# Kernel tuning notes

Hardware: AMD Instinct MI355X
Metric: run time of the kernel (lower is better)

## Reference

```python
import jax, jax.numpy as jnp
import numpy as np

N = 50000
E = 800000
HEADS = 4
C = 64  # per-head channels
IN = 256
NEG_SLOPE = 0.2


def setup_inputs() -> dict:
    key = jax.random.key(0)
    k = jax.random.split(key, 6)
    x = jax.random.normal(k[0], (N, IN), dtype=jnp.float32)
    edge_index = jax.random.randint(k[1], (2, E), 0, N, dtype=jnp.int64)
    # Glorot-ish scale for weights
    W = jax.random.normal(k[2], (IN, HEADS * C), dtype=jnp.float32) * (1.0 / np.sqrt(IN))
    att_src = jax.random.normal(k[3], (HEADS, C), dtype=jnp.float32) * (1.0 / np.sqrt(C))
    att_dst = jax.random.normal(k[4], (HEADS, C), dtype=jnp.float32) * (1.0 / np.sqrt(C))
    bias = jax.random.normal(k[5], (HEADS * C,), dtype=jnp.float32) * 0.02
    return {"x": x, "edge_index": edge_index, "W": W, "att_src": att_src,
            "att_dst": att_dst, "bias": bias}


def _gat_forward(x, edge_index, W, att_src, att_dst, bias):
    n = x.shape[0]
    h = (x @ W).reshape(n, HEADS, C)  # [N, H, C]

    # add self loops (PyG default add_self_loops=True)
    loop = jnp.arange(n, dtype=edge_index.dtype)
    src = jnp.concatenate([edge_index[0], loop])  # [E+N]
    dst = jnp.concatenate([edge_index[1], loop])

    # per-node attention contributions  [N, H]
    a_src = jnp.einsum('nhc,hc->nh', h, att_src)
    a_dst = jnp.einsum('nhc,hc->nh', h, att_dst)

    # edge logits with leaky relu  [E+N, H]
    logits = a_src[src] + a_dst[dst]
    logits = jnp.where(logits >= 0, logits, NEG_SLOPE * logits)

    # segment softmax over destination neighborhoods
    seg_max = jax.ops.segment_max(logits, dst, num_segments=n)  # [N, H]
    seg_max = jnp.where(jnp.isfinite(seg_max), seg_max, 0.0)
    ex = jnp.exp(logits - seg_max[dst])
    denom = jax.ops.segment_sum(ex, dst, num_segments=n)  # [N, H]
    alpha = ex / (denom[dst] + 1e-16)  # [E+N, H]

    # weighted scatter-add of source messages
    msgs = alpha[:, :, None] * h[src]  # [E+N, H, C]
    out = jax.ops.segment_sum(msgs, dst, num_segments=n)  # [N, H, C]
    out = out.reshape(n, HEADS * C) + bias
    return jax.nn.relu(out)


def reference(x, edge_index, W, att_src, att_dst, bias):
    return _gat_forward(x, edge_index, W, att_src, att_dst, bias)
```

## Files before the change

### kernel.cpp

```cpp
#include <hip/hip_runtime.h>
#include <hip/hip_bf16.h>
#include <math.h>

#define NEG 0.2f
#define BSH 6
#define EPB 2048

typedef __attribute__((ext_vector_type(4))) float f4;
typedef __attribute__((ext_vector_type(8))) short s8;

__device__ __forceinline__ short f2bf(float f) {
    unsigned u = __float_as_uint(f);
    u += 0x7fff + ((u >> 16) & 1);
    return (short)(u >> 16);
}
__device__ __forceinline__ unsigned pk2(float a, float b) {
    union { __hip_bfloat162 h; unsigned u; } c;
    c.h = __float22bfloat162_rn(make_float2(a, b));
    return c.u;
}
__device__ __forceinline__ float bf2f(unsigned short s) {
    return __uint_as_float(((unsigned)s) << 16);
}

__global__ __launch_bounds__(256) void prep_count(
    const float* __restrict__ W, short* __restrict__ Wt, int* __restrict__ off,
    const int* __restrict__ ei, int* __restrict__ hist2d,
    int E, int N, int NBUCK, int NB, int Etot)
{
    const int blk = blockIdx.x, t = threadIdx.x;
    if (blk < 256) {
        int id = blk * 256 + t;
        int n = id >> 8, k = id & 255;
        Wt[id] = f2bf(W[k * 256 + n]);
        if (id == 0) off[N] = Etot;
        return;
    }
    extern __shared__ int lh[];
    const int cblk = blk - 256;
    for (int b = t; b < NBUCK; b += 256) lh[b] = 0;
    __syncthreads();
    const int e0 = cblk * EPB;
    if (e0 + EPB <= E) {
#pragma unroll
        for (int i = 0; i < EPB / 1024; ++i) {
            int e = e0 + i * 1024 + t * 4;
            int4 d = *(const int4*)(ei + E + e);
            atomicAdd(&lh[d.x >> BSH], 1);
            atomicAdd(&lh[d.y >> BSH], 1);
            atomicAdd(&lh[d.z >> BSH], 1);
            atomicAdd(&lh[d.w >> BSH], 1);
        }
    } else {
        for (int i = 0; i < EPB / 256; ++i) {
            int e = e0 + i * 256 + t;
            if (e < Etot) {
                int dte = (e < E) ? ei[E + e] : (e - E);
                atomicAdd(&lh[dte >> BSH], 1);
            }
        }
    }
    __syncthreads();
    for (int b = t; b < NBUCK; b += 256) hist2d[b * NB + cblk] = lh[b];
}

__global__ __launch_bounds__(1024) void scan1(const int* __restrict__ src,
                                              int* __restrict__ dst,
                                              int* __restrict__ bsum, int Ntot)
{
    __shared__ int wsum[16], wexc[16];
    const int t = threadIdx.x, lane = t & 63, w = t >> 6;
    const int idx = blockIdx.x * 1024 + t;
    int v = (idx < Ntot) ? src[idx] : 0;
    int val = v;
#pragma unroll
    for (int o = 1; o < 64; o <<= 1) {
        int u = __shfl_up(val, o);
        if (lane >= o) val += u;
    }
    if (lane == 63) wsum[w] = val;
    __syncthreads();
    if (t < 16) {
        int s = wsum[t];
#pragma unroll
        for (int o = 1; o < 16; o <<= 1) {
            int u = __shfl_up(s, o, 16);
            if (t >= o) s += u;
        }
        wexc[t] = s - wsum[t];
        if (t == 15) bsum[blockIdx.x] = s;
    }
    __syncthreads();
    if (idx < Ntot) dst[idx] = wexc[w] + val - v;
}

__global__ __launch_bounds__(1024) void scan2v(const int* __restrict__ bsum,
                                               int* __restrict__ bexc, int nb)
{
    __shared__ int wsum[16], wexc[16];
    const int t = threadIdx.x, lane = t & 63, w = t >> 6;
    int v = (t < nb) ? bsum[t] : 0;
    int val = v;
#pragma unroll
    for (int o = 1; o < 64; o <<= 1) {
        int u = __shfl_up(val, o);
        if (lane >= o) val += u;
    }
    if (lane == 63) wsum[w] = val;
    __syncthreads();
    if (t < 16) {
        int s = wsum[t];
#pragma unroll
        for (int o = 1; o < 16; o <<= 1) {
            int u = __shfl_up(s, o, 16);
            if (t >= o) s += u;
        }
        wexc[t] = s - wsum[t];
    }
    __syncthreads();
    if (t < nb) bexc[t] = wexc[w] + val - v;
}

__global__ __launch_bounds__(512) void gemm_scatter(
    const float* __restrict__ x, const short* __restrict__ Wt,
    const float* __restrict__ att_src, const float* __restrict__ att_dst,
    short* __restrict__ hb, float* __restrict__ a_src_n,
    float* __restrict__ a_dst_n, int M, int GB,
    const int* __restrict__ ei, const int* __restrict__ scanned,
    const int* __restrict__ bexc, unsigned* __restrict__ bucketed,
    int E, int N, int NBUCK, int NB)
{
    extern __shared__ __align__(16) char smem[];
    const int t = threadIdx.x;

    if (blockIdx.x >= GB) {
        int* lcur = (int*)smem;
        const int cblk = blockIdx.x - GB;
        for (int b = t; b < NBUCK; b += 512) {
            int idx = b * NB + cblk;
            lcur[b] = scanned[idx] + bexc[idx >> 10];
        }
        __syncthreads();
        const int e0 = cblk * EPB, Etot = E + N;
        if (e0 + EPB <= E) {
            int e = e0 + t * 4;
            int4 s4 = *(const int4*)(ei + e);
            int4 d4 = *(const int4*)(ei + E + e);
            int p0 = atomicAdd(&lcur[d4.x >> BSH], 1);
            bucketed[p0] = (unsigned)s4.x | ((unsigned)(d4.x & 63) << 20);
            int p1 = atomicAdd(&lcur[d4.y >> BSH], 1);
            bucketed[p1] = (unsigned)s4.y | ((unsigned)(d4.y & 63) << 20);
            int p2 = atomicAdd(&lcur[d4.z >> BSH], 1);
            bucketed[p2] = (unsigned)s4.z | ((unsigned)(d4.z & 63) << 20);
            int p3 = atomicAdd(&lcur[d4.w >> BSH], 1);
            bucketed[p3] = (unsigned)s4.w | ((unsigned)(d4.w & 63) << 20);
        } else {
            for (int i = 0; i < EPB / 512; ++i) {
                int e = e0 + i * 512 + t;
                if (e < Etot) {
                    int src, dte;
                    if (e < E) { src = ei[e]; dte = ei[E + e]; }
                    else       { src = e - E; dte = src; }
                    int pos = atomicAdd(&lcur[dte >> BSH], 1);
                    bucketed[pos] = (unsigned)src | ((unsigned)(dte & 63) << 20);
                }
            }
        }
        return;
    }

    short (*xs)[128][32] = (short (*)[128][32])smem;
    const int lane = t & 63, wv = t >> 6;
    const int wr = wv >> 2;
    const int hd = wv & 3;
    const int quad = lane >> 4, l15 = lane & 15;
    const int n0 = blockIdx.x * 128;

    const int row = t >> 2, kq = t & 3;
    const bool okr = (n0 + row) < M;
    const float* xp = x + (size_t)(n0 + row) * 256 + kq * 8;

    const short* wbase = Wt + (size_t)(hd * 64 + l15) * 256 + quad * 8;

    f4 acc[4][4];
#pragma unroll
    for (int i = 0; i < 4; ++i)
#pragma unroll
        for (int j = 0; j < 4; ++j) acc[i][j] = (f4)(0.f);

    float4 v0 = {}, v1 = {};
    if (okr) { const float4* p = (const float4*)xp; v0 = p[0]; v1 = p[1]; }

    s8 af[4];
#pragma unroll
    for (int i = 0; i < 4; ++i)
        af[i] = *(const s8*)(wbase + (size_t)(i * 16) * 256);

    int buf = 0;
#pragma unroll
    for (int ks = 0; ks < 8; ++ks) {
        uint4 u = { pk2(v0.x, v0.y), pk2(v0.z, v0.w), pk2(v1.x, v1.y), pk2(v1.z, v1.w) };
        *(uint4*)&xs[buf][row][kq * 8] = u;
        __syncthreads();

        if (ks < 7 && okr) {
            const float4* p = (const float4*)(xp + (ks + 1) * 32);
            v0 = p[0]; v1 = p[1];
        }

        s8 afn[4];
        if (ks < 7) {
#pragma unroll
            for (int i = 0; i < 4; ++i)
                afn[i] = *(const s8*)(wbase + (size_t)(i * 16) * 256 + (ks + 1) * 32);
        }

        s8 bf[4];
#pragma unroll
        for (int j = 0; j < 4; ++j)
            bf[j] = *(const s8*)&xs[buf][wr * 64 + j * 16 + l15][quad * 8];
#pragma unroll
        for (int i = 0; i < 4; ++i)
#pragma unroll
            for (int j = 0; j < 4; ++j)
                acc[i][j] = __builtin_amdgcn_mfma_f32_16x16x32_bf16(af[i], bf[j], acc[i][j], 0, 0, 0);

        if (ks < 7) {
#pragma unroll
            for (int i = 0; i < 4; ++i) af[i] = afn[i];
        }
        buf ^= 1;
    }

    float asv[4][4], adv[4][4];
#pragma unroll
    for (int i = 0; i < 4; ++i)
#pragma unroll
        for (int rr = 0; rr < 4; ++rr) {
            asv[i][rr] = att_src[hd * 64 + i * 16 + quad * 4 + rr];
            adv[i][rr] = att_dst[hd * 64 + i * 16 + quad * 4 + rr];
        }

#pragma unroll
    for (int j = 0; j < 4; ++j) {
        const int node = n0 + wr * 64 + j * 16 + l15;
        const bool ok = node < M;
        float ps = 0.f, pd = 0.f;
#pragma unroll
        for (int i = 0; i < 4; ++i)
#pragma unroll
            for (int rr = 0; rr < 4; ++rr) {
                float v = acc[i][j][rr];
                ps = fmaf(v, asv[i][rr], ps);
                pd = fmaf(v, adv[i][rr], pd);
            }
        ps += __shfl_xor(ps, 16); ps += __shfl_xor(ps, 32);
        pd += __shfl_xor(pd, 16); pd += __shfl_xor(pd, 32);
        if (ok && quad == 0) {
            a_src_n[node * 4 + hd] = ps;
            a_dst_n[node * 4 + hd] = pd;
        }
        if (ok) {
#pragma unroll
            for (int i = 0; i < 4; ++i) {
                uint2 pk = make_uint2(pk2(acc[i][j][0], acc[i][j][1]),
                                      pk2(acc[i][j][2], acc[i][j][3]));
                *(uint2*)&hb[(size_t)node * 256 + hd * 64 + i * 16 + quad * 4] = pk;
            }
        }
    }
}

__global__ __launch_bounds__(256) void csr_build(
    const unsigned* __restrict__ bucketed, const int* __restrict__ scanned,
    const int* __restrict__ bexc, int* __restrict__ off, int* __restrict__ csr,
    int N, int NB, int NBUCK, int Etot)
{
    __shared__ unsigned est[2048];
    __shared__ int ldeg4[4][64], lcur4[4][64], loff[64];
    const int t = threadIdx.x, wv = t >> 6, b = blockIdx.x;

    const int i0 = b * NB;
    const int gbase = scanned[i0] + bexc[i0 >> 10];
    int gend;
    if (b + 1 == NBUCK) gend = Etot;
    else { int i1 = (b + 1) * NB; gend = scanned[i1] + bexc[i1 >> 10]; }
    int cnt = gend - gbase;
    if (cnt > 2048) cnt = 2048;

    ldeg4[t >> 6][t & 63] = 0;
    __syncthreads();
    for (int i = t; i < cnt; i += 256) {
        unsigned en = bucketed[gbase + i];
        est[i] = en;
        atomicAdd(&ldeg4[wv][en >> 20], 1);
    }
    __syncthreads();
    if (t < 64) {
        int d0 = ldeg4[0][t], d1 = ldeg4[1][t], d2 = ldeg4[2][t], d3 = ldeg4[3][t];
        int tot = d0 + d1 + d2 + d3;
        int val = tot;
#pragma unroll
        for (int o = 1; o < 64; o <<= 1) {
            int u = __shfl_up(val, o);
            if (t >= o) val += u;
        }
        int excl = val - tot;
        loff[t] = excl;
        lcur4[0][t] = excl;
        lcur4[1][t] = excl + d0;
        lcur4[2][t] = excl + d0 + d1;
        lcur4[3][t] = excl + d0 + d1 + d2;
    }
    __syncthreads();
    for (int i = t; i < cnt; i += 256) {
        unsigned en = est[i];
        int pos = atomicAdd(&lcur4[wv][en >> 20], 1);
        csr[gbase + pos] = (int)(en & 0xFFFFF);
    }
    if (t < 64) {
        int n = (b << BSH) + t;
        if (n < N) off[n] = gbase + loff[t];
    }
}

__global__ __launch_bounds__(256) void aggregate(const short* __restrict__ hb,
                                                 const float* __restrict__ a_src_n,
                                                 const float* __restrict__ a_dst_n,
                                                 const int* __restrict__ off,
                                                 const int* __restrict__ csr,
                                                 const float* __restrict__ bias,
                                                 float* __restrict__ out, int N)
{
    __shared__ float lds_w[4][64][4];
    __shared__ int   lds_s[4][64];
    const int wv = threadIdx.x >> 6;
    const int lane = threadIdx.x & 63;
    const int half = lane >> 5, l31 = lane & 31;
    const int n = blockIdx.x * 4 + wv;
    if (n >= N) return;

    const int base = off[n];
    const int d = off[n + 1] - base;
    const float4 ad = *(const float4*)(a_dst_n + 4 * n);
    const int hl = l31 >> 3;

    float acc[8] = {0.f, 0.f, 0.f, 0.f, 0.f, 0.f, 0.f, 0.f};
    float4 sum = make_float4(0.f, 0.f, 0.f, 0.f);
    const uint4* hp = (const uint4*)hb;

    for (int c0 = 0; c0 < d; c0 += 64) {
        int j = c0 + lane;
        int s = 0;
        float4 w4 = make_float4(0.f, 0.f, 0.f, 0.f);
        if (j < d) {
            s = csr[base + j];
            float4 as = *(const float4*)(a_src_n + 4 * s);
            float lx = as.x + ad.x; lx = lx >= 0.f ? lx : NEG * lx;
            float ly = as.y + ad.y; ly = ly >= 0.f ? ly : NEG * ly;
            float lz = as.z + ad.z; lz = lz >= 0.f ? lz : NEG * lz;
            float lw = as.w + ad.w; lw = lw >= 0.f ? lw : NEG * lw;
            w4 = make_float4(__expf(lx), __expf(ly), __expf(lz), __expf(lw));
        }
        sum.x += w4.x; sum.y += w4.y; sum.z += w4.z; sum.w += w4.w;
        *(float4*)&lds_w[wv][lane][0] = w4;
        lds_s[wv][lane] = s;
        __builtin_amdgcn_wave_barrier();

        const int cl = (d - c0) < 64 ? (d - c0) : 64;
        int jj = 0;
        for (; jj + 4 <= cl; jj += 4) {
            int   s0 = lds_s[wv][jj + half];
            int   s1 = lds_s[wv][jj + 2 + half];
            float w0 = lds_w[wv][jj + half][hl];
            float w1 = lds_w[wv][jj + 2 + half][hl];
            uint4 v0 = hp[(size_t)s0 * 32 + l31];
            uint4 v1 = hp[(size_t)s1 * 32 + l31];
            acc[0] = fmaf(w0, bf2f((unsigned short)(v0.x & 0xffff)), acc[0]);
            acc[1] = fmaf(w0, bf2f((unsigned short)(v0.x >> 16)),    acc[1]);
            acc[2] = fmaf(w0, bf2f((unsigned short)(v0.y & 0xffff)), acc[2]);
            acc[3] = fmaf(w0, bf2f((unsigned short)(v0.y >> 16)),    acc[3]);
            acc[4] = fmaf(w0, bf2f((unsigned short)(v0.z & 0xffff)), acc[4]);
            acc[5] = fmaf(w0, bf2f((unsigned short)(v0.z >> 16)),    acc[5]);
            acc[6] = fmaf(w0, bf2f((unsigned short)(v0.w & 0xffff)), acc[6]);
            acc[7] = fmaf(w0, bf2f((unsigned short)(v0.w >> 16)),    acc[7]);
            acc[0] = fmaf(w1, bf2f((unsigned short)(v1.x & 0xffff)), acc[0]);
            acc[1] = fmaf(w1, bf2f((unsigned short)(v1.x >> 16)),    acc[1]);
            acc[2] = fmaf(w1, bf2f((unsigned short)(v1.y & 0xffff)), acc[2]);
            acc[3] = fmaf(w1, bf2f((unsigned short)(v1.y >> 16)),    acc[3]);
            acc[4] = fmaf(w1, bf2f((unsigned short)(v1.z & 0xffff)), acc[4]);
            acc[5] = fmaf(w1, bf2f((unsigned short)(v1.z >> 16)),    acc[5]);
            acc[6] = fmaf(w1, bf2f((unsigned short)(v1.w & 0xffff)), acc[6]);
            acc[7] = fmaf(w1, bf2f((unsigned short)(v1.w >> 16)),    acc[7]);
        }
        for (; jj < cl; jj += 2) {
            int   s0 = lds_s[wv][jj + half];
            float w0 = lds_w[wv][jj + half][hl];
            uint4 v0 = hp[(size_t)s0 * 32 + l31];
            acc[0] = fmaf(w0, bf2f((unsigned short)(v0.x & 0xffff)), acc[0]);
            acc[1] = fmaf(w0, bf2f((unsigned short)(v0.x >> 16)),    acc[1]);
            acc[2] = fmaf(w0, bf2f((unsigned short)(v0.y & 0xffff)), acc[2]);
            acc[3] = fmaf(w0, bf2f((unsigned short)(v0.y >> 16)),    acc[3]);
            acc[4] = fmaf(w0, bf2f((unsigned short)(v0.z & 0xffff)), acc[4]);
            acc[5] = fmaf(w0, bf2f((unsigned short)(v0.z >> 16)),    acc[5]);
            acc[6] = fmaf(w0, bf2f((unsigned short)(v0.w & 0xffff)), acc[6]);
            acc[7] = fmaf(w0, bf2f((unsigned short)(v0.w >> 16)),    acc[7]);
        }
        __builtin_amdgcn_wave_barrier();
    }

#pragma unroll
    for (int k = 0; k < 8; ++k) acc[k] += __shfl_xor(acc[k], 32);

#pragma unroll
    for (int o = 32; o > 0; o >>= 1) {
        sum.x += __shfl_xor(sum.x, o);
        sum.y += __shfl_xor(sum.y, o);
        sum.z += __shfl_xor(sum.z, o);
        sum.w += __shfl_xor(sum.w, o);
    }
    float sh = (hl & 2) ? ((hl & 1) ? sum.w : sum.z) : ((hl & 1) ? sum.y : sum.x);
    float ih = 1.f / (sh + 1e-16f);

    if (half == 0) {
        const float4* bp = (const float4*)bias + l31 * 2;
        float4 b0 = bp[0], b1 = bp[1];
        float4 o0, o1;
        o0.x = fmaxf(fmaf(acc[0], ih, b0.x), 0.f);
        o0.y = fmaxf(fmaf(acc[1], ih, b0.y), 0.f);
        o0.z = fmaxf(fmaf(acc[2], ih, b0.z), 0.f);
        o0.w = fmaxf(fmaf(acc[3], ih, b0.w), 0.f);
        o1.x = fmaxf(fmaf(acc[4], ih, b1.x), 0.f);
        o1.y = fmaxf(fmaf(acc[5], ih, b1.y), 0.f);
        o1.z = fmaxf(fmaf(acc[6], ih, b1.z), 0.f);
        o1.w = fmaxf(fmaf(acc[7], ih, b1.w), 0.f);
        float4* op = (float4*)(out + (size_t)n * 256) + l31 * 2;
        op[0] = o0;
        op[1] = o1;
    }
}

extern "C" void kernel_launch(void* const* d_in, const int* in_sizes, int n_in,
                              void* d_out, int out_size, void* d_ws, size_t ws_size,
                              hipStream_t stream)
{
    const float* x       = (const float*)d_in[0];
    const int*   ei      = (const int*)d_in[1];
    const float* W       = (const float*)d_in[2];
    const float* att_src = (const float*)d_in[3];
    const float* att_dst = (const float*)d_in[4];
    const float* bias    = (const float*)d_in[5];
    float* out = (float*)d_out;

    const int N = in_sizes[0] / 256;
    const int E = in_sizes[1] / 2;
    const int Etot = E + N;
    const int NBUCK = (N + 63) >> BSH;
    const int NB = (Etot + EPB - 1) / EPB;
    const int Ntot = NBUCK * NB;
    const int nb1 = (Ntot + 1023) / 1024;
    const int GB = (N + 127) / 128;

    char* p = (char*)d_ws;
    short*    hb      = (short*)p;    p += (size_t)N * 256 * sizeof(short);
    short*    Wt      = (short*)p;    p += 256 * 256 * sizeof(short);
    float*    a_src_n = (float*)p;    p += (size_t)N * 4 * sizeof(float);
    float*    a_dst_n = (float*)p;    p += (size_t)N * 4 * sizeof(float);
    int*      hist2d  = (int*)p;      p += (size_t)Ntot * sizeof(int);
    int*      scanned = (int*)p;      p += (size_t)Ntot * sizeof(int);
    int*      bsum    = (int*)p;      p += 1024 * sizeof(int);
    int*      bexc    = (int*)p;      p += 1024 * sizeof(int);
    int*      off     = (int*)p;      p += (size_t)(N + 1) * sizeof(int);
    unsigned* bucketed= (unsigned*)p; p += (size_t)Etot * sizeof(unsigned);
    int*      csr     = (int*)p;      p += (size_t)Etot * sizeof(int);

    prep_count<<<256 + NB, 256, NBUCK * sizeof(int), stream>>>(
        W, Wt, off, ei, hist2d, E, N, NBUCK, NB, Etot);
    scan1<<<nb1, 1024, 0, stream>>>(hist2d, scanned, bsum, Ntot);
    scan2v<<<1, 1024, 0, stream>>>(bsum, bexc, nb1);
    gemm_scatter<<<GB + NB, 512, 16384, stream>>>(
        x, Wt, att_src, att_dst, hb, a_src_n, a_dst_n, N, GB,
        ei, scanned, bexc, bucketed, E, N, NBUCK, NB);
    csr_build<<<NBUCK, 256, 0, stream>>>(bucketed, scanned, bexc, off, csr,
                                         N, NB, NBUCK, Etot);
    aggregate<<<(N + 3) / 4, 256, 0, stream>>>(hb, a_src_n, a_dst_n, off, csr,
                                               bias, out, N);
}
```

Before: 215.1 us.

## Replace per-block histogram scan with per-bucket scan and global atomic cursors

The edge bucketing no longer computes a prefix scan over a full bucket-by-block histogram. A single-block kernel now sums each bucket's counts across coarser histogram blocks and scans the totals into bucket bases and cursors. The scatter phase claims slots with global atomics on those shared cursors, which removes one scan kernel and most of the histogram traffic. The cost is heavy L2 atomic contention on about 800 counters, and edges land in a nondeterministic order within each bucket.

```diff
diff --git a/kernel.cpp b/kernel.cpp
--- a/kernel.cpp
+++ b/kernel.cpp
@@ -4,7 +4,8 @@
 
 #define NEG 0.2f
 #define BSH 6
-#define EPB 2048
+#define EPB_H 8192
+#define EPB_S 2048
 
 typedef __attribute__((ext_vector_type(4))) float f4;
 typedef __attribute__((ext_vector_type(8))) short s8;
@@ -26,7 +27,7 @@
 __global__ __launch_bounds__(256) void prep_count(
     const float* __restrict__ W, short* __restrict__ Wt, int* __restrict__ off,
     const int* __restrict__ ei, int* __restrict__ hist2d,
-    int E, int N, int NBUCK, int NB, int Etot)
+    int E, int N, int NBUCK, int Etot)
 {
     const int blk = blockIdx.x, t = threadIdx.x;
     if (blk < 256) {
@@ -40,10 +41,10 @@
     const int cblk = blk - 256;
     for (int b = t; b < NBUCK; b += 256) lh[b] = 0;
     __syncthreads();
-    const int e0 = cblk * EPB;
-    if (e0 + EPB <= E) {
-#pragma unroll
-        for (int i = 0; i < EPB / 1024; ++i) {
+    const int e0 = cblk * EPB_H;
+    if (e0 + EPB_H <= E) {
+#pragma unroll
+        for (int i = 0; i < EPB_H / 1024; ++i) {
             int e = e0 + i * 1024 + t * 4;
             int4 d = *(const int4*)(ei + E + e);
             atomicAdd(&lh[d.x >> BSH], 1);
@@ -52,7 +53,7 @@
             atomicAdd(&lh[d.w >> BSH], 1);
         }
     } else {
-        for (int i = 0; i < EPB / 256; ++i) {
+        for (int i = 0; i < EPB_H / 256; ++i) {
             int e = e0 + i * 256 + t;
             if (e < Etot) {
                 int dte = (e < E) ? ei[E + e] : (e - E);
@@ -61,17 +62,22 @@
         }
     }
     __syncthreads();
-    for (int b = t; b < NBUCK; b += 256) hist2d[b * NB + cblk] = lh[b];
-}
-
-__global__ __launch_bounds__(1024) void scan1(const int* __restrict__ src,
-                                              int* __restrict__ dst,
-                                              int* __restrict__ bsum, int Ntot)
+    for (int b = t; b < NBUCK; b += 256)
+        hist2d[(size_t)cblk * NBUCK + b] = lh[b];
+}
+
+__global__ __launch_bounds__(1024) void scan_small(const int* __restrict__ hist2d,
+                                                   int* __restrict__ bbase,
+                                                   int* __restrict__ bcur,
+                                                   int NBUCK, int NBH)
 {
     __shared__ int wsum[16], wexc[16];
     const int t = threadIdx.x, lane = t & 63, w = t >> 6;
-    const int idx = blockIdx.x * 1024 + t;
-    int v = (idx < Ntot) ? src[idx] : 0;
+    int v = 0;
+    if (t < NBUCK) {
+        const int* col = hist2d + t;
+        for (int r = 0; r < NBH; ++r) v += col[(size_t)r * NBUCK];
+    }
     int val = v;
 #pragma unroll
     for (int o = 1; o < 64; o <<= 1) {
@@ -88,37 +94,11 @@
             if (t >= o) s += u;
         }
         wexc[t] = s - wsum[t];
-        if (t == 15) bsum[blockIdx.x] = s;
-    }
-    __syncthreads();
-    if (idx < Ntot) dst[idx] = wexc[w] + val - v;
-}
-
-__global__ __launch_bounds__(1024) void scan2v(const int* __restrict__ bsum,
-                                               int* __restrict__ bexc, int nb)
-{
-    __shared__ int wsum[16], wexc[16];
-    const int t = threadIdx.x, lane = t & 63, w = t >> 6;
-    int v = (t < nb) ? bsum[t] : 0;
-    int val = v;
-#pragma unroll
-    for (int o = 1; o < 64; o <<= 1) {
-        int u = __shfl_up(val, o);
-        if (lane >= o) val += u;
-    }
-    if (lane == 63) wsum[w] = val;
-    __syncthreads();
-    if (t < 16) {
-        int s = wsum[t];
-#pragma unroll
-        for (int o = 1; o < 16; o <<= 1) {
-            int u = __shfl_up(s, o, 16);
-            if (t >= o) s += u;
-        }
-        wexc[t] = s - wsum[t];
-    }
-    __syncthreads();
-    if (t < nb) bexc[t] = wexc[w] + val - v;
+    }
+    __syncthreads();
+    int excl = wexc[w] + val - v;
+    if (t < NBUCK) { bbase[t] = excl; bcur[t] = excl; }
+    if (t == NBUCK) bbase[t] = excl;
 }
 
 __global__ __launch_bounds__(512) void gemm_scatter(
@@ -126,42 +106,35 @@
     const float* __restrict__ att_src, const float* __restrict__ att_dst,
     short* __restrict__ hb, float* __restrict__ a_src_n,
     float* __restrict__ a_dst_n, int M, int GB,
-    const int* __restrict__ ei, const int* __restrict__ scanned,
-    const int* __restrict__ bexc, unsigned* __restrict__ bucketed,
-    int E, int N, int NBUCK, int NB)
+    const int* __restrict__ ei, int* __restrict__ bcur,
+    unsigned* __restrict__ bucketed, int E, int N)
 {
     extern __shared__ __align__(16) char smem[];
     const int t = threadIdx.x;
 
     if (blockIdx.x >= GB) {
-        int* lcur = (int*)smem;
         const int cblk = blockIdx.x - GB;
-        for (int b = t; b < NBUCK; b += 512) {
-            int idx = b * NB + cblk;
-            lcur[b] = scanned[idx] + bexc[idx >> 10];
-        }
-        __syncthreads();
-        const int e0 = cblk * EPB, Etot = E + N;
-        if (e0 + EPB <= E) {
+        const int e0 = cblk * EPB_S, Etot = E + N;
+        if (e0 + EPB_S <= E) {
             int e = e0 + t * 4;
             int4 s4 = *(const int4*)(ei + e);
             int4 d4 = *(const int4*)(ei + E + e);
-            int p0 = atomicAdd(&lcur[d4.x >> BSH], 1);
+            int p0 = atomicAdd(&bcur[d4.x >> BSH], 1);
             bucketed[p0] = (unsigned)s4.x | ((unsigned)(d4.x & 63) << 20);
-            int p1 = atomicAdd(&lcur[d4.y >> BSH], 1);
+            int p1 = atomicAdd(&bcur[d4.y >> BSH], 1);
             bucketed[p1] = (unsigned)s4.y | ((unsigned)(d4.y & 63) << 20);
-            int p2 = atomicAdd(&lcur[d4.z >> BSH], 1);
+            int p2 = atomicAdd(&bcur[d4.z >> BSH], 1);
             bucketed[p2] = (unsigned)s4.z | ((unsigned)(d4.z & 63) << 20);
-            int p3 = atomicAdd(&lcur[d4.w >> BSH], 1);
+            int p3 = atomicAdd(&bcur[d4.w >> BSH], 1);
             bucketed[p3] = (unsigned)s4.w | ((unsigned)(d4.w & 63) << 20);
         } else {
-            for (int i = 0; i < EPB / 512; ++i) {
+            for (int i = 0; i < EPB_S / 512; ++i) {
                 int e = e0 + i * 512 + t;
                 if (e < Etot) {
                     int src, dte;
                     if (e < E) { src = ei[e]; dte = ei[E + e]; }
                     else       { src = e - E; dte = src; }
-                    int pos = atomicAdd(&lcur[dte >> BSH], 1);
+                    int pos = atomicAdd(&bcur[dte >> BSH], 1);
                     bucketed[pos] = (unsigned)src | ((unsigned)(dte & 63) << 20);
                 }
             }
@@ -272,19 +245,16 @@
 }
 
 __global__ __launch_bounds__(256) void csr_build(
-    const unsigned* __restrict__ bucketed, const int* __restrict__ scanned,
-    const int* __restrict__ bexc, int* __restrict__ off, int* __restrict__ csr,
-    int N, int NB, int NBUCK, int Etot)
+    const unsigned* __restrict__ bucketed, const int* __restrict__ bbase,
+    int* __restrict__ off, int* __restrict__ csr,
+    int N, int NBUCK, int Etot)
 {
     __shared__ unsigned est[2048];
     __shared__ int ldeg4[4][64], lcur4[4][64], loff[64];
     const int t = threadIdx.x, wv = t >> 6, b = blockIdx.x;
 
-    const int i0 = b * NB;
-    const int gbase = scanned[i0] + bexc[i0 >> 10];
-    int gend;
-    if (b + 1 == NBUCK) gend = Etot;
-    else { int i1 = (b + 1) * NB; gend = scanned[i1] + bexc[i1 >> 10]; }
+    const int gbase = bbase[b];
+    const int gend  = bbase[b + 1];
     int cnt = gend - gbase;
     if (cnt > 2048) cnt = 2048;
 
@@ -456,9 +426,8 @@
     const int E = in_sizes[1] / 2;
     const int Etot = E + N;
     const int NBUCK = (N + 63) >> BSH;
-    const int NB = (Etot + EPB - 1) / EPB;
-    const int Ntot = NBUCK * NB;
-    const int nb1 = (Ntot + 1023) / 1024;
+    const int NBH = (Etot + EPB_H - 1) / EPB_H;
+    const int NBS = (Etot + EPB_S - 1) / EPB_S;
     const int GB = (N + 127) / 128;
 
     char* p = (char*)d_ws;
@@ -466,23 +435,21 @@
     short*    Wt      = (short*)p;    p += 256 * 256 * sizeof(short);
     float*    a_src_n = (float*)p;    p += (size_t)N * 4 * sizeof(float);
     float*    a_dst_n = (float*)p;    p += (size_t)N * 4 * sizeof(float);
-    int*      hist2d  = (int*)p;      p += (size_t)Ntot * sizeof(int);
-    int*      scanned = (int*)p;      p += (size_t)Ntot * sizeof(int);
-    int*      bsum    = (int*)p;      p += 1024 * sizeof(int);
-    int*      bexc    = (int*)p;      p += 1024 * sizeof(int);
+    int*      hist2d  = (int*)p;      p += (size_t)NBH * NBUCK * sizeof(int);
+    int*      bbase   = (int*)p;      p += (size_t)(NBUCK + 1) * sizeof(int);
+    int*      bcur    = (int*)p;      p += (size_t)NBUCK * sizeof(int);
     int*      off     = (int*)p;      p += (size_t)(N + 1) * sizeof(int);
     unsigned* bucketed= (unsigned*)p; p += (size_t)Etot * sizeof(unsigned);
     int*      csr     = (int*)p;      p += (size_t)Etot * sizeof(int);
 
-    prep_count<<<256 + NB, 256, NBUCK * sizeof(int), stream>>>(
-        W, Wt, off, ei, hist2d, E, N, NBUCK, NB, Etot);
-    scan1<<<nb1, 1024, 0, stream>>>(hist2d, scanned, bsum, Ntot);
-    scan2v<<<1, 1024, 0, stream>>>(bsum, bexc, nb1);
-    gemm_scatter<<<GB + NB, 512, 16384, stream>>>(
+    prep_count<<<256 + NBH, 256, NBUCK * sizeof(int), stream>>>(
+        W, Wt, off, ei, hist2d, E, N, NBUCK, Etot);
+    scan_small<<<1, 1024, 0, stream>>>(hist2d, bbase, bcur, NBUCK, NBH);
+    gemm_scatter<<<GB + NBS, 512, 16384, stream>>>(
         x, Wt, att_src, att_dst, hb, a_src_n, a_dst_n, N, GB,
-        ei, scanned, bexc, bucketed, E, N, NBUCK, NB);
-    csr_build<<<NBUCK, 256, 0, stream>>>(bucketed, scanned, bexc, off, csr,
-                                         N, NB, NBUCK, Etot);
+        ei, bcur, bucketed, E, N);
+    csr_build<<<NBUCK, 256, 0, stream>>>(bucketed, bbase, off, csr,
+                                         N, NBUCK, Etot);
     aggregate<<<(N + 3) / 4, 256, 0, stream>>>(hb, a_src_n, a_dst_n, off, csr,
                                                bias, out, N);
 }
```

New measurement: 439.1 us. 104% more time.
